# Kernel optimization log

Measured on AMD Instinct MI355X. Metric: run time of the kernel, lower is better.

Reference implementation:

```python
import jax, jax.numpy as jnp
import numpy as np

N_HEAD = 16

def setup_inputs() -> dict:
    key = jax.random.key(0)
    ks = jax.random.split(key, 5)
    B, T, C = 2, 2048, 1024
    s = 1.0 / np.sqrt(C)
    return {
        "x":  jax.random.normal(ks[0], (B, T, C), jnp.float32),
        "Wk": jax.random.normal(ks[1], (C, C), jnp.float32) * s,
        "Wq": jax.random.normal(ks[2], (C, C), jnp.float32) * s,
        "Wv": jax.random.normal(ks[3], (C, C), jnp.float32) * s,
        "Wp": jax.random.normal(ks[4], (C, C), jnp.float32) * s,
    }

def reference(x, Wk, Wq, Wv, Wp):
    B, T, C = x.shape
    H = N_HEAD
    D = C // H
    # torch Linear (bias=False): y = x @ W.T
    def proj(W):
        return (x @ W.T).reshape(B, T, H, D).transpose(0, 2, 1, 3)  # [B,H,T,D]
    q, k, v = proj(Wq), proj(Wk), proj(Wv)
    att = jnp.einsum("bhtd,bhsd->bhts", q, k) / jnp.sqrt(jnp.float32(D))
    causal = jnp.tril(jnp.ones((T, T), dtype=bool))
    att = jnp.where(causal[None, None], att, -jnp.inf)
    att = jax.nn.softmax(att, axis=-1)
    y = jnp.einsum("bhts,bhsd->bhtd", att, v)
    y = y.transpose(0, 2, 1, 3).reshape(B, T, C)
    return y @ Wp.T
```

## Files before the change

kernel.cpp:

```cpp
#include <hip/hip_runtime.h>

typedef unsigned short u16;
typedef unsigned int u32;
typedef unsigned long long u64;
typedef __attribute__((ext_vector_type(8))) short bf16x8;
typedef __attribute__((ext_vector_type(8))) _Float16 f16x8;
typedef __attribute__((ext_vector_type(4))) float f32x4;
typedef __attribute__((ext_vector_type(4))) u32 u32x4;

#define GLOAD16(gp, lp) __builtin_amdgcn_global_load_lds( \
  (const __attribute__((address_space(1))) unsigned int*)(gp), \
  (__attribute__((address_space(3))) unsigned int*)(lp), 16, 0, 0)

__device__ __forceinline__ u16 f2bf(float f) {
  unsigned int u = __builtin_bit_cast(unsigned int, f);
  u += 0x7fffu + ((u >> 16) & 1u);
  return (u16)(u >> 16);
}

__device__ __forceinline__ u32 pk2(float a, float b) {
  return (u32)f2bf(a) | ((u32)f2bf(b) << 16);
}

__device__ __forceinline__ u32 pkh(float a, float b) {
  return __builtin_bit_cast(u32, __builtin_amdgcn_cvt_pkrtz(a, b));
}

__device__ __forceinline__ void wait_barrier() {
  asm volatile("s_waitcnt vmcnt(0)" ::: "memory");
  __builtin_amdgcn_s_barrier();
  __builtin_amdgcn_sched_barrier(0);
}

__global__ __launch_bounds__(256) void cvt_all(
    const float* __restrict__ x,
    const float* __restrict__ w0, const float* __restrict__ w1,
    const float* __restrict__ w2, const float* __restrict__ w3,
    u16* __restrict__ ox, u16* __restrict__ o0, u16* __restrict__ o1,
    u16* __restrict__ o2, u16* __restrict__ o3) {
  int bid = blockIdx.x;
  const float* in; u16* out; size_t off;
  if (bid < 4096) {
    in = x; out = ox; off = (size_t)bid << 10;
  } else {
    int r = bid - 4096, z = r >> 10;
    in  = (z == 0) ? w0 : (z == 1) ? w1 : (z == 2) ? w2 : w3;
    out = (z == 0) ? o0 : (z == 1) ? o1 : (z == 2) ? o2 : o3;
    off = (size_t)(r & 1023) << 10;
  }
  size_t i = off + (size_t)threadIdx.x * 4;
  float4 f = *reinterpret_cast<const float4*>(in + i);
  u64 v = (u64)pk2(f.x, f.y) | ((u64)pk2(f.z, f.w) << 32);
  *reinterpret_cast<u64*>(out + i) = v;
}

template<int MODE, int MI>
__device__ __forceinline__ void gemm_bt_body(
    const u16* __restrict__ A, const u16* __restrict__ Bw, void* __restrict__ Cout,
    int m0, int n0, float scale) {
  const int K = 1024;
  __shared__ __align__(16) u16 As[2][MI * 32 * 32];
  __shared__ __align__(16) u16 Bs[2][128 * 32];
  const int tid = threadIdx.x;
  const int lane = tid & 63, wid = tid >> 6;
  const int wr = wid >> 1, wc = wid & 1;
  const int g = lane >> 4, c = lane & 15;
  f32x4 acc[MI][4] = {};

  auto stage = [&](int buf, int k0) {
#pragma unroll
    for (int i = 0; i < MI / 2; ++i) {
      int idx = tid + i * 256;
      int row = idx >> 2, slot = idx & 3;
      int ss = slot ^ (row & 3);
      GLOAD16(A + (size_t)(m0 + row) * K + k0 + ss * 8, &As[buf][idx * 8]);
    }
#pragma unroll
    for (int i = 0; i < 2; ++i) {
      int idx = tid + i * 256;
      int row = idx >> 2, slot = idx & 3;
      int ss = slot ^ (row & 3);
      GLOAD16(Bw + (size_t)(n0 + row) * K + k0 + ss * 8, &Bs[buf][idx * 8]);
    }
  };

  stage(0, 0);
  int buf = 0;
#pragma unroll 1
  for (int kt = 0; kt < 32; ++kt) {
    wait_barrier();
    if (kt + 1 < 32) stage(buf ^ 1, (kt + 1) * 32);
    bf16x8 af[MI], bfr[4];
#pragma unroll
    for (int mi = 0; mi < MI; ++mi) {
      int row = wr * (MI * 16) + mi * 16 + c;
      int slot = g ^ (row & 3);
      af[mi] = *(const bf16x8*)&As[buf][row * 32 + slot * 8];
    }
#pragma unroll
    for (int ni = 0; ni < 4; ++ni) {
      int row = wc * 64 + ni * 16 + c;
      int slot = g ^ (row & 3);
      bfr[ni] = *(const bf16x8*)&Bs[buf][row * 32 + slot * 8];
    }
    __builtin_amdgcn_s_setprio(1);
#pragma unroll
    for (int mi = 0; mi < MI; ++mi)
#pragma unroll
      for (int ni = 0; ni < 4; ++ni)
        acc[mi][ni] = __builtin_amdgcn_mfma_f32_16x16x32_bf16(af[mi], bfr[ni], acc[mi][ni], 0, 0, 0);
    __builtin_amdgcn_s_setprio(0);
    buf ^= 1;
  }

#pragma unroll
  for (int mi = 0; mi < MI; ++mi)
#pragma unroll
    for (int ni = 0; ni < 4; ++ni)
#pragma unroll
      for (int i = 0; i < 4; ++i) {
        int m = m0 + wr * (MI * 16) + mi * 16 + g * 4 + i;
        int n = n0 + wc * 64 + ni * 16 + c;
        float v = acc[mi][ni][i];
        if (MODE == 0) {
          int b = m >> 11, t = m & 2047, h = n >> 6, d = n & 63;
          ((u16*)Cout)[(((size_t)b * 16 + h) * 2048 + t) * 64 + d] = f2bf(v * scale);
        } else {
          ((float*)Cout)[(size_t)m * 1024 + n] = v;
        }
      }
}

#define QSCALE 0.1803368801111204f

__global__ __launch_bounds__(256, 3) void proj_qkv(
    const u16* __restrict__ xb, const u16* __restrict__ wq, const u16* __restrict__ wk,
    const u16* __restrict__ wv, u16* __restrict__ q, u16* __restrict__ k, u16* __restrict__ v) {
  int z = blockIdx.z;
  const u16* W = (z == 0) ? wq : (z == 1) ? wk : wv;
  u16* O = (z == 0) ? q : (z == 1) ? k : v;
  float scale = (z == 0) ? QSCALE : 1.0f;
  gemm_bt_body<0, 4>(xb, W, O, blockIdx.y * 128, blockIdx.x * 128, scale);
}

__global__ __launch_bounds__(256, 2) void gemm_out(
    const u16* __restrict__ y, const u16* __restrict__ wp, float* __restrict__ out) {
  gemm_bt_body<1, 2>(y, wp, out, blockIdx.y * 64, blockIdx.x * 128, 1.0f);
}

__global__ __launch_bounds__(256) void transpose_v_kernel(
    const u16* __restrict__ v, u16* __restrict__ vt) {
  __shared__ u16 tile[64][65];
  int bh = blockIdx.y, t0 = blockIdx.x * 64;
  const u16* src = v + ((size_t)bh * 2048 + t0) * 64;
  u16* dst = vt + (size_t)bh * 64 * 2048 + t0;
  int tid = threadIdx.x;
#pragma unroll
  for (int i = 0; i < 16; ++i) {
    int idx = tid + i * 256;
    tile[idx >> 6][idx & 63] = src[idx];
  }
  __syncthreads();
#pragma unroll
  for (int i = 0; i < 16; ++i) {
    int idx = tid + i * 256;
    int d = idx >> 6, j = idx & 63;
    int t = (((((j >> 2) & 1) << 1) | (j >> 5)) << 4) | (((j >> 3) & 3) << 2) | (j & 3);
    float f = __builtin_bit_cast(float, (u32)tile[t][d] << 16);
    _Float16 hh = (_Float16)f;
    dst[(size_t)d * 2048 + j] = __builtin_bit_cast(u16, hh);
  }
}

__global__ __launch_bounds__(256, 4) void attn_kernel(
    const u16* __restrict__ q, const u16* __restrict__ kg,
    const u16* __restrict__ vt, u16* __restrict__ y) {
  const int T = 2048;
  __shared__ __align__(16) u16 Ks[2][64 * 64];
  __shared__ __align__(16) u16 Vs[2][64 * 64];
  const int tid = threadIdx.x, lane = tid & 63, w = tid >> 6;
  const int g = lane >> 4, c = lane & 15;
  const int bh = blockIdx.x;
  const int yy = blockIdx.y, m8 = yy >> 3, o8 = yy & 7;
  const int qt = (m8 == 0) ? o8 : (m8 == 1) ? 31 - o8 : (m8 == 2) ? 8 + o8 : 23 - o8;
  const u16* Q = q + (size_t)bh * T * 64;
  const u16* K = kg + (size_t)bh * T * 64;
  const u16* V = vt + (size_t)bh * 64 * T;
  const int b = bh >> 4, h = bh & 15;
  const int qrow0 = qt * 64 + w * 16;

  f16x8 ones;
#pragma unroll
  for (int j = 0; j < 8; ++j) ones[j] = (_Float16)1.0f;

  auto stage = [&](int bb, int j0) {
#pragma unroll
    for (int i = 0; i < 2; ++i) {
      int idx = tid + i * 256;
      int row = idx >> 3, slot = idx & 7;
      int ss = slot ^ (row & 7);
      GLOAD16(K + (size_t)(j0 + row) * 64 + ss * 8, &Ks[bb][idx * 8]);
      GLOAD16(V + (size_t)row * T + j0 + ss * 8, &Vs[bb][idx * 8]);
    }
  };

  bf16x8 qf[2];
#pragma unroll
  for (int kk = 0; kk < 2; ++kk)
    qf[kk] = *(const bf16x8*)&Q[(size_t)(qrow0 + c) * 64 + kk * 32 + g * 8];

  f32x4 o[4] = {};
  f32x4 ol = {};

  const int nkt = qt + 1;
  stage(0, 0);
  int buf = 0;
#pragma unroll 1
  for (int kt = 0; kt < nkt; ++kt) {
    const int j0 = kt * 64;
    wait_barrier();
    if (kt + 1 < nkt) stage(buf ^ 1, j0 + 64);

    bf16x8 kb[4][2];
#pragma unroll
    for (int ni = 0; ni < 4; ++ni)
#pragma unroll
      for (int kk = 0; kk < 2; ++kk) {
        int kr = ni * 16 + c;
        int slot = (kk * 4 + g) ^ (kr & 7);
        kb[ni][kk] = *(const bf16x8*)&Ks[buf][kr * 64 + slot * 8];
      }
    f32x4 s[4];
    __builtin_amdgcn_s_setprio(1);
#pragma unroll
    for (int ni = 0; ni < 4; ++ni) {
      f32x4 a = {0.f, 0.f, 0.f, 0.f};
      a = __builtin_amdgcn_mfma_f32_16x16x32_bf16(kb[ni][0], qf[0], a, 0, 0, 0);
      a = __builtin_amdgcn_mfma_f32_16x16x32_bf16(kb[ni][1], qf[1], a, 0, 0, 0);
      s[ni] = a;
    }
    __builtin_amdgcn_s_setprio(0);

    const bool dumask = (kt == qt);
#pragma unroll
    for (int ni = 0; ni < 4; ++ni)
#pragma unroll
      for (int i = 0; i < 4; ++i) {
        float val = s[ni][i];
        if (dumask) {
          int key = j0 + ni * 16 + g * 4 + i;
          if (key > qrow0 + c) val = -3.0e38f;
        }
        s[ni][i] = __builtin_amdgcn_exp2f(val);
      }

    u32x4 pa0 = { pkh(s[0][0], s[0][1]), pkh(s[0][2], s[0][3]),
                  pkh(s[2][0], s[2][1]), pkh(s[2][2], s[2][3]) };
    u32x4 pa1 = { pkh(s[1][0], s[1][1]), pkh(s[1][2], s[1][3]),
                  pkh(s[3][0], s[3][1]), pkh(s[3][2], s[3][3]) };
    f16x8 pa[2];
    pa[0] = __builtin_bit_cast(f16x8, pa0);
    pa[1] = __builtin_bit_cast(f16x8, pa1);

    f16x8 vb[4][2];
#pragma unroll
    for (int di = 0; di < 4; ++di)
#pragma unroll
      for (int kk = 0; kk < 2; ++kk) {
        int d = di * 16 + c;
        int slot = (kk * 4 + g) ^ (d & 7);
        vb[di][kk] = *(const f16x8*)&Vs[buf][d * 64 + slot * 8];
      }
    __builtin_amdgcn_s_setprio(1);
    ol = __builtin_amdgcn_mfma_f32_16x16x32_f16(pa[0], ones, ol, 0, 0, 0);
    ol = __builtin_amdgcn_mfma_f32_16x16x32_f16(pa[1], ones, ol, 0, 0, 0);
#pragma unroll
    for (int di = 0; di < 4; ++di) {
      o[di] = __builtin_amdgcn_mfma_f32_16x16x32_f16(pa[0], vb[di][0], o[di], 0, 0, 0);
      o[di] = __builtin_amdgcn_mfma_f32_16x16x32_f16(pa[1], vb[di][1], o[di], 0, 0, 0);
    }
    __builtin_amdgcn_s_setprio(0);
    buf ^= 1;
  }

#pragma unroll
  for (int i = 0; i < 4; ++i) {
    float inv = 1.f / ol[i];
    int t = qrow0 + g * 4 + i;
#pragma unroll
    for (int di = 0; di < 4; ++di) {
      int col = h * 64 + di * 16 + c;
      y[((size_t)b * 2048 + t) * 1024 + col] = f2bf(o[di][i] * inv);
    }
  }
}

extern "C" void kernel_launch(void* const* d_in, const int* in_sizes, int n_in,
                              void* d_out, int out_size, void* d_ws, size_t ws_size,
                              hipStream_t stream) {
  const float* x  = (const float*)d_in[0];
  const float* Wk = (const float*)d_in[1];
  const float* Wq = (const float*)d_in[2];
  const float* Wv = (const float*)d_in[3];
  const float* Wp = (const float*)d_in[4];
  float* out = (float*)d_out;

  char* ws = (char*)d_ws;
  const size_t SZ_X = (size_t)4096 * 1024 * 2;
  const size_t SZ_W = (size_t)1024 * 1024 * 2;
  u16* xb  = (u16*)(ws);
  u16* qb  = (u16*)(ws + SZ_X);
  u16* kb  = (u16*)(ws + 2 * SZ_X);
  u16* vb  = (u16*)(ws + 3 * SZ_X);
  u16* wqb = (u16*)(ws + 4 * SZ_X);
  u16* wkb = (u16*)(ws + 4 * SZ_X + SZ_W);
  u16* wvb = (u16*)(ws + 4 * SZ_X + 2 * SZ_W);
  u16* wpb = (u16*)(ws + 4 * SZ_X + 3 * SZ_W);

  cvt_all<<<8192, 256, 0, stream>>>(x, Wq, Wk, Wv, Wp, xb, wqb, wkb, wvb, wpb);

  proj_qkv<<<dim3(8, 32, 3), 256, 0, stream>>>(xb, wqb, wkb, wvb, qb, kb, vb);

  u16* vtb = xb;
  transpose_v_kernel<<<dim3(32, 32), 256, 0, stream>>>(vb, vtb);

  u16* yb = vb;
  attn_kernel<<<dim3(32, 32), 256, 0, stream>>>(qb, kb, vtb, yb);

  gemm_out<<<dim3(8, 64), 256, 0, stream>>>(yb, wpb, out);
}
```

Measured before the change: 110.7 us.

## Enlarge attention query tile to 128 rows with two row-blocks per wave

```diff
diff --git a/kernel.cpp b/kernel.cpp
--- a/kernel.cpp
+++ b/kernel.cpp
@@ -172,7 +172,7 @@
   }
 }
 
-__global__ __launch_bounds__(256, 4) void attn_kernel(
+__global__ __launch_bounds__(256, 2) void attn_kernel(
     const u16* __restrict__ q, const u16* __restrict__ kg,
     const u16* __restrict__ vt, u16* __restrict__ y) {
   const int T = 2048;
@@ -181,13 +181,13 @@
   const int tid = threadIdx.x, lane = tid & 63, w = tid >> 6;
   const int g = lane >> 4, c = lane & 15;
   const int bh = blockIdx.x;
-  const int yy = blockIdx.y, m8 = yy >> 3, o8 = yy & 7;
-  const int qt = (m8 == 0) ? o8 : (m8 == 1) ? 31 - o8 : (m8 == 2) ? 8 + o8 : 23 - o8;
+  const int yy = blockIdx.y;
+  const int qt = (yy < 8) ? (15 - yy) : (yy - 8);
   const u16* Q = q + (size_t)bh * T * 64;
   const u16* K = kg + (size_t)bh * T * 64;
   const u16* V = vt + (size_t)bh * 64 * T;
   const int b = bh >> 4, h = bh & 15;
-  const int qrow0 = qt * 64 + w * 16;
+  const int qrow0 = qt * 128 + w * 32;
 
   f16x8 ones;
 #pragma unroll
@@ -204,15 +204,17 @@
     }
   };
 
-  bf16x8 qf[2];
-#pragma unroll
-  for (int kk = 0; kk < 2; ++kk)
-    qf[kk] = *(const bf16x8*)&Q[(size_t)(qrow0 + c) * 64 + kk * 32 + g * 8];
-
-  f32x4 o[4] = {};
-  f32x4 ol = {};
-
-  const int nkt = qt + 1;
+  bf16x8 qf[2][2];
+#pragma unroll
+  for (int r = 0; r < 2; ++r)
+#pragma unroll
+    for (int kk = 0; kk < 2; ++kk)
+      qf[r][kk] = *(const bf16x8*)&Q[(size_t)(qrow0 + r * 16 + c) * 64 + kk * 32 + g * 8];
+
+  f32x4 o[2][4] = {};
+  f32x4 ol[2] = {};
+
+  const int nkt = qt * 2 + 2;
   stage(0, 0);
   int buf = 0;
 #pragma unroll 1
@@ -230,37 +232,44 @@
         int slot = (kk * 4 + g) ^ (kr & 7);
         kb[ni][kk] = *(const bf16x8*)&Ks[buf][kr * 64 + slot * 8];
       }
-    f32x4 s[4];
+    f32x4 s[2][4];
     __builtin_amdgcn_s_setprio(1);
 #pragma unroll
-    for (int ni = 0; ni < 4; ++ni) {
-      f32x4 a = {0.f, 0.f, 0.f, 0.f};
-      a = __builtin_amdgcn_mfma_f32_16x16x32_bf16(kb[ni][0], qf[0], a, 0, 0, 0);
-      a = __builtin_amdgcn_mfma_f32_16x16x32_bf16(kb[ni][1], qf[1], a, 0, 0, 0);
-      s[ni] = a;
-    }
+    for (int r = 0; r < 2; ++r)
+#pragma unroll
+      for (int ni = 0; ni < 4; ++ni) {
+        f32x4 a = {0.f, 0.f, 0.f, 0.f};
+        a = __builtin_amdgcn_mfma_f32_16x16x32_bf16(kb[ni][0], qf[r][0], a, 0, 0, 0);
+        a = __builtin_amdgcn_mfma_f32_16x16x32_bf16(kb[ni][1], qf[r][1], a, 0, 0, 0);
+        s[r][ni] = a;
+      }
     __builtin_amdgcn_s_setprio(0);
 
-    const bool dumask = (kt == qt);
-#pragma unroll
-    for (int ni = 0; ni < 4; ++ni)
-#pragma unroll
-      for (int i = 0; i < 4; ++i) {
-        float val = s[ni][i];
-        if (dumask) {
-          int key = j0 + ni * 16 + g * 4 + i;
-          if (key > qrow0 + c) val = -3.0e38f;
+    const bool dumask = (j0 + 63 > qrow0);
+#pragma unroll
+    for (int r = 0; r < 2; ++r)
+#pragma unroll
+      for (int ni = 0; ni < 4; ++ni)
+#pragma unroll
+        for (int i = 0; i < 4; ++i) {
+          float val = s[r][ni][i];
+          if (dumask) {
+            int key = j0 + ni * 16 + g * 4 + i;
+            if (key > qrow0 + r * 16 + c) val = -3.0e38f;
+          }
+          s[r][ni][i] = __builtin_amdgcn_exp2f(val);
         }
-        s[ni][i] = __builtin_amdgcn_exp2f(val);
-      }
-
-    u32x4 pa0 = { pkh(s[0][0], s[0][1]), pkh(s[0][2], s[0][3]),
-                  pkh(s[2][0], s[2][1]), pkh(s[2][2], s[2][3]) };
-    u32x4 pa1 = { pkh(s[1][0], s[1][1]), pkh(s[1][2], s[1][3]),
-                  pkh(s[3][0], s[3][1]), pkh(s[3][2], s[3][3]) };
-    f16x8 pa[2];
-    pa[0] = __builtin_bit_cast(f16x8, pa0);
-    pa[1] = __builtin_bit_cast(f16x8, pa1);
+
+    f16x8 pa[2][2];
+#pragma unroll
+    for (int r = 0; r < 2; ++r) {
+      u32x4 p0 = { pkh(s[r][0][0], s[r][0][1]), pkh(s[r][0][2], s[r][0][3]),
+                   pkh(s[r][2][0], s[r][2][1]), pkh(s[r][2][2], s[r][2][3]) };
+      u32x4 p1 = { pkh(s[r][1][0], s[r][1][1]), pkh(s[r][1][2], s[r][1][3]),
+                   pkh(s[r][3][0], s[r][3][1]), pkh(s[r][3][2], s[r][3][3]) };
+      pa[r][0] = __builtin_bit_cast(f16x8, p0);
+      pa[r][1] = __builtin_bit_cast(f16x8, p1);
+    }
 
     f16x8 vb[4][2];
 #pragma unroll
@@ -272,27 +281,34 @@
         vb[di][kk] = *(const f16x8*)&Vs[buf][d * 64 + slot * 8];
       }
     __builtin_amdgcn_s_setprio(1);
-    ol = __builtin_amdgcn_mfma_f32_16x16x32_f16(pa[0], ones, ol, 0, 0, 0);
-    ol = __builtin_amdgcn_mfma_f32_16x16x32_f16(pa[1], ones, ol, 0, 0, 0);
-#pragma unroll
-    for (int di = 0; di < 4; ++di) {
-      o[di] = __builtin_amdgcn_mfma_f32_16x16x32_f16(pa[0], vb[di][0], o[di], 0, 0, 0);
-      o[di] = __builtin_amdgcn_mfma_f32_16x16x32_f16(pa[1], vb[di][1], o[di], 0, 0, 0);
-    }
+#pragma unroll
+    for (int r = 0; r < 2; ++r) {
+      ol[r] = __builtin_amdgcn_mfma_f32_16x16x32_f16(pa[r][0], ones, ol[r], 0, 0, 0);
+      ol[r] = __builtin_amdgcn_mfma_f32_16x16x32_f16(pa[r][1], ones, ol[r], 0, 0, 0);
+    }
+#pragma unroll
+    for (int di = 0; di < 4; ++di)
+#pragma unroll
+      for (int r = 0; r < 2; ++r) {
+        o[r][di] = __builtin_amdgcn_mfma_f32_16x16x32_f16(pa[r][0], vb[di][0], o[r][di], 0, 0, 0);
+        o[r][di] = __builtin_amdgcn_mfma_f32_16x16x32_f16(pa[r][1], vb[di][1], o[r][di], 0, 0, 0);
+      }
     __builtin_amdgcn_s_setprio(0);
     buf ^= 1;
   }
 
 #pragma unroll
-  for (int i = 0; i < 4; ++i) {
-    float inv = 1.f / ol[i];
-    int t = qrow0 + g * 4 + i;
-#pragma unroll
-    for (int di = 0; di < 4; ++di) {
-      int col = h * 64 + di * 16 + c;
-      y[((size_t)b * 2048 + t) * 1024 + col] = f2bf(o[di][i] * inv);
-    }
-  }
+  for (int r = 0; r < 2; ++r)
+#pragma unroll
+    for (int i = 0; i < 4; ++i) {
+      float inv = 1.f / ol[r][i];
+      int t = qrow0 + r * 16 + g * 4 + i;
+#pragma unroll
+      for (int di = 0; di < 4; ++di) {
+        int col = h * 64 + di * 16 + c;
+        y[((size_t)b * 2048 + t) * 1024 + col] = f2bf(o[r][di][i] * inv);
+      }
+    }
 }
 
 extern "C" void kernel_launch(void* const* d_in, const int* in_sizes, int n_in,
@@ -325,7 +341,7 @@
   transpose_v_kernel<<<dim3(32, 32), 256, 0, stream>>>(vb, vtb);
 
   u16* yb = vb;
-  attn_kernel<<<dim3(32, 32), 256, 0, stream>>>(qb, kb, vtb, yb);
+  attn_kernel<<<dim3(32, 16), 256, 0, stream>>>(qb, kb, vtb, yb);
 
   gemm_out<<<dim3(8, 64), 256, 0, stream>>>(yb, wpb, out);
 }
```

After: 121.4 us. 9.7% more time.

## Fuse x fp32-to-bf16 conversion into QKV projection GEMM A-tile loads

Applied to the files above, without the earlier changes.

```diff
diff --git a/kernel.cpp b/kernel.cpp
--- a/kernel.cpp
+++ b/kernel.cpp
@@ -32,34 +32,26 @@
   __builtin_amdgcn_sched_barrier(0);
 }
 
-__global__ __launch_bounds__(256) void cvt_all(
-    const float* __restrict__ x,
+__global__ __launch_bounds__(256) void cvt_w4(
     const float* __restrict__ w0, const float* __restrict__ w1,
     const float* __restrict__ w2, const float* __restrict__ w3,
-    u16* __restrict__ ox, u16* __restrict__ o0, u16* __restrict__ o1,
+    u16* __restrict__ o0, u16* __restrict__ o1,
     u16* __restrict__ o2, u16* __restrict__ o3) {
-  int bid = blockIdx.x;
-  const float* in; u16* out; size_t off;
-  if (bid < 4096) {
-    in = x; out = ox; off = (size_t)bid << 10;
-  } else {
-    int r = bid - 4096, z = r >> 10;
-    in  = (z == 0) ? w0 : (z == 1) ? w1 : (z == 2) ? w2 : w3;
-    out = (z == 0) ? o0 : (z == 1) ? o1 : (z == 2) ? o2 : o3;
-    off = (size_t)(r & 1023) << 10;
-  }
-  size_t i = off + (size_t)threadIdx.x * 4;
+  int z = blockIdx.y;
+  const float* in = (z == 0) ? w0 : (z == 1) ? w1 : (z == 2) ? w2 : w3;
+  u16* out = (z == 0) ? o0 : (z == 1) ? o1 : (z == 2) ? o2 : o3;
+  int i = (blockIdx.x * 256 + threadIdx.x) * 4;
   float4 f = *reinterpret_cast<const float4*>(in + i);
   u64 v = (u64)pk2(f.x, f.y) | ((u64)pk2(f.z, f.w) << 32);
   *reinterpret_cast<u64*>(out + i) = v;
 }
 
-template<int MODE, int MI>
+template<int MODE, int MI, int AF32>
 __device__ __forceinline__ void gemm_bt_body(
-    const u16* __restrict__ A, const u16* __restrict__ Bw, void* __restrict__ Cout,
+    const void* __restrict__ Av, const u16* __restrict__ Bw, void* __restrict__ Cout,
     int m0, int n0, float scale) {
   const int K = 1024;
-  __shared__ __align__(16) u16 As[2][MI * 32 * 32];
+  __shared__ __align__(16) u16 As[2][MI * 32 * 32 * (AF32 ? 2 : 1)];
   __shared__ __align__(16) u16 Bs[2][128 * 32];
   const int tid = threadIdx.x;
   const int lane = tid & 63, wid = tid >> 6;
@@ -68,12 +60,25 @@
   f32x4 acc[MI][4] = {};
 
   auto stage = [&](int buf, int k0) {
-#pragma unroll
-    for (int i = 0; i < MI / 2; ++i) {
-      int idx = tid + i * 256;
-      int row = idx >> 2, slot = idx & 3;
-      int ss = slot ^ (row & 3);
-      GLOAD16(A + (size_t)(m0 + row) * K + k0 + ss * 8, &As[buf][idx * 8]);
+    if (AF32) {
+      const float* A = (const float*)Av;
+#pragma unroll
+      for (int i = 0; i < MI; ++i) {
+        int idx = tid + i * 256;
+        int row = idx >> 3, slot = idx & 7;
+        int ss = slot ^ (row & 7);
+        GLOAD16(A + (size_t)(m0 + row) * K + k0 + ss * 4,
+                ((float*)&As[buf][0]) + idx * 4);
+      }
+    } else {
+      const u16* A = (const u16*)Av;
+#pragma unroll
+      for (int i = 0; i < MI / 2; ++i) {
+        int idx = tid + i * 256;
+        int row = idx >> 2, slot = idx & 3;
+        int ss = slot ^ (row & 3);
+        GLOAD16(A + (size_t)(m0 + row) * K + k0 + ss * 8, &As[buf][idx * 8]);
+      }
     }
 #pragma unroll
     for (int i = 0; i < 2; ++i) {
@@ -94,8 +99,19 @@
 #pragma unroll
     for (int mi = 0; mi < MI; ++mi) {
       int row = wr * (MI * 16) + mi * 16 + c;
-      int slot = g ^ (row & 3);
-      af[mi] = *(const bf16x8*)&As[buf][row * 32 + slot * 8];
+      if (AF32) {
+        const float* Ab = (const float*)&As[buf][0];
+        int s0 = (g * 2) ^ (row & 7);
+        int s1 = (g * 2 + 1) ^ (row & 7);
+        f32x4 lo = *(const f32x4*)(Ab + row * 32 + s0 * 4);
+        f32x4 hi = *(const f32x4*)(Ab + row * 32 + s1 * 4);
+        u32x4 p = { pk2(lo[0], lo[1]), pk2(lo[2], lo[3]),
+                    pk2(hi[0], hi[1]), pk2(hi[2], hi[3]) };
+        af[mi] = __builtin_bit_cast(bf16x8, p);
+      } else {
+        int slot = g ^ (row & 3);
+        af[mi] = *(const bf16x8*)&As[buf][row * 32 + slot * 8];
+      }
     }
 #pragma unroll
     for (int ni = 0; ni < 4; ++ni) {
@@ -134,18 +150,18 @@
 #define QSCALE 0.1803368801111204f
 
 __global__ __launch_bounds__(256, 3) void proj_qkv(
-    const u16* __restrict__ xb, const u16* __restrict__ wq, const u16* __restrict__ wk,
+    const float* __restrict__ x, const u16* __restrict__ wq, const u16* __restrict__ wk,
     const u16* __restrict__ wv, u16* __restrict__ q, u16* __restrict__ k, u16* __restrict__ v) {
   int z = blockIdx.z;
   const u16* W = (z == 0) ? wq : (z == 1) ? wk : wv;
   u16* O = (z == 0) ? q : (z == 1) ? k : v;
   float scale = (z == 0) ? QSCALE : 1.0f;
-  gemm_bt_body<0, 4>(xb, W, O, blockIdx.y * 128, blockIdx.x * 128, scale);
+  gemm_bt_body<0, 4, 1>(x, W, O, blockIdx.y * 128, blockIdx.x * 128, scale);
 }
 
 __global__ __launch_bounds__(256, 2) void gemm_out(
     const u16* __restrict__ y, const u16* __restrict__ wp, float* __restrict__ out) {
-  gemm_bt_body<1, 2>(y, wp, out, blockIdx.y * 64, blockIdx.x * 128, 1.0f);
+  gemm_bt_body<1, 2, 0>(y, wp, out, blockIdx.y * 64, blockIdx.x * 128, 1.0f);
 }
 
 __global__ __launch_bounds__(256) void transpose_v_kernel(
@@ -308,20 +324,19 @@
   char* ws = (char*)d_ws;
   const size_t SZ_X = (size_t)4096 * 1024 * 2;
   const size_t SZ_W = (size_t)1024 * 1024 * 2;
-  u16* xb  = (u16*)(ws);
+  u16* vb  = (u16*)(ws);
   u16* qb  = (u16*)(ws + SZ_X);
   u16* kb  = (u16*)(ws + 2 * SZ_X);
-  u16* vb  = (u16*)(ws + 3 * SZ_X);
+  u16* vtb = (u16*)(ws + 3 * SZ_X);
   u16* wqb = (u16*)(ws + 4 * SZ_X);
   u16* wkb = (u16*)(ws + 4 * SZ_X + SZ_W);
   u16* wvb = (u16*)(ws + 4 * SZ_X + 2 * SZ_W);
   u16* wpb = (u16*)(ws + 4 * SZ_X + 3 * SZ_W);
 
-  cvt_all<<<8192, 256, 0, stream>>>(x, Wq, Wk, Wv, Wp, xb, wqb, wkb, wvb, wpb);
-
-  proj_qkv<<<dim3(8, 32, 3), 256, 0, stream>>>(xb, wqb, wkb, wvb, qb, kb, vb);
-
-  u16* vtb = xb;
+  cvt_w4<<<dim3(1024, 4), 256, 0, stream>>>(Wq, Wk, Wv, Wp, wqb, wkb, wvb, wpb);
+
+  proj_qkv<<<dim3(8, 32, 3), 256, 0, stream>>>(x, wqb, wkb, wvb, qb, kb, vb);
+
   transpose_v_kernel<<<dim3(32, 32), 256, 0, stream>>>(vb, vtb);
 
   u16* yb = vb;
```

Result: slower. 117.1 us (+5.8%).
